# Performance work log

Hardware: AMD Instinct MI355X
Metric: run time of the kernel (lower is better)

## Reference

```python
import jax, jax.numpy as jnp
import numpy as np

HEADS = 8
DIM_HEAD = 128
BUCKET_SIZE = 128


def setup_inputs() -> dict:
    key = jax.random.key(0)
    ks = jax.random.split(key, 5)
    b, t, d = 4, 4096, 1024
    dh_all = HEADS * DIM_HEAD  # 1024
    x = jax.random.normal(ks[0], (b, t, d), dtype=jnp.float32)
    # 0.02 init scale keeps qk logits in a sane range (mimics trained-weight scale)
    Wq = jax.random.normal(ks[1], (d, dh_all), dtype=jnp.float32) * 0.02
    Wkv = jax.random.normal(ks[2], (d, 2 * dh_all), dtype=jnp.float32) * 0.02
    Wo = jax.random.normal(ks[3], (dh_all, d), dtype=jnp.float32) * 0.02
    bo = jnp.zeros((d,), dtype=jnp.float32)
    return {"x": x, "Wq": Wq, "Wkv": Wkv, "Wo": Wo, "bo": bo}


def reference(x, Wq, Wkv, Wo, bo):
    b, t, d = x.shape
    h, dh, bs = HEADS, DIM_HEAD, BUCKET_SIZE
    buckets = t // bs
    scale = dh ** -0.5

    # projections (Linear without bias for q/kv)
    q = x @ Wq                      # [b, t, h*dh]
    k, v = jnp.split(x @ Wkv, 2, axis=-1)

    def merge_heads(u):             # [b, t, h*dh] -> [b*h, t, dh]
        return u.reshape(b, t, h, dh).transpose(0, 2, 1, 3).reshape(b * h, t, dh)

    q, k, v = merge_heads(q), merge_heads(k), merge_heads(v)

    # bucket: [b*h, buckets, bs, dh]
    bq = q.reshape(b * h, buckets, bs, dh)
    bk = k.reshape(b * h, buckets, bs, dh)
    bv = v.reshape(b * h, buckets, bs, dh)

    # AttentionSortNet (non_permutative=True): bucket-mean similarity -> softmax
    sq = bq.mean(axis=2)            # [b*h, buckets, dh]
    sk = bk.mean(axis=2)
    R = jnp.einsum('bie,bje->bij', sq, sk) * scale
    R = jax.nn.softmax(R, axis=-1)  # [b*h, buckets, buckets]

    # soft-reorder kv buckets and concat with local buckets (n_sortcut == 0)
    bk_r = jnp.einsum('buv,bvtd->butd', R, bk)
    bv_r = jnp.einsum('buv,bvtd->butd', R, bv)
    bk_cat = jnp.concatenate([bk_r, bk], axis=2)   # [b*h, buckets, 2*bs, dh]
    bv_cat = jnp.concatenate([bv_r, bv], axis=2)

    # per-bucket attention
    dots = jnp.einsum('buie,buje->buij', bq, bk_cat) * scale
    attn = jax.nn.softmax(dots, axis=-1)
    out = jnp.einsum('buij,buje->buie', attn, bv_cat)  # [b*h, buckets, bs, dh]

    # unbucket + split heads back: [b, t, h*dh]
    out = out.reshape(b, h, t, dh).transpose(0, 2, 1, 3).reshape(b, t, h * dh)
    return out @ Wo + bo
```

## Files before the change

### kernel.cpp

```cpp
#include <hip/hip_runtime.h>
#include <hip/hip_bf16.h>
#include <stdint.h>

typedef short short8 __attribute__((ext_vector_type(8)));
typedef float f32x4 __attribute__((ext_vector_type(4)));
typedef float f32x2 __attribute__((ext_vector_type(2)));

__device__ __forceinline__ unsigned short f2bf(float f) {
    unsigned u = __float_as_uint(f);
    u += 0x7fff + ((u >> 16) & 1);
    return (unsigned short)(u >> 16);
}
__device__ __forceinline__ float bf2f(unsigned short h) {
    return __uint_as_float(((unsigned)h) << 16);
}

__device__ __forceinline__ void gload_lds16(const void* g, void* l) {
    __builtin_amdgcn_global_load_lds(
        (const __attribute__((address_space(1))) void*)g,
        (__attribute__((address_space(3))) void*)l, 16, 0, 0);
}

__global__ void cast_x_kernel(const float* __restrict__ x, unsigned short* __restrict__ xb, int n) {
    int i = (blockIdx.x * blockDim.x + threadIdx.x) * 4;
    int stride = gridDim.x * blockDim.x * 4;
    for (; i < n; i += stride) {
        float4 f = *(const float4*)(x + i);
        ushort4 o;
        o.x = f2bf(f.x); o.y = f2bf(f.y); o.z = f2bf(f.z); o.w = f2bf(f.w);
        *(ushort4*)(xb + i) = o;
    }
}

__global__ void transpose_cast_kernel(const float* __restrict__ W, unsigned short* __restrict__ Wt,
                                      int K, int N) {
    __shared__ unsigned short tile[32][33];
    int k0 = blockIdx.x * 32, n0 = blockIdx.y * 32;
    int tx = threadIdx.x & 31, ty = threadIdx.x >> 5;
#pragma unroll
    for (int i = 0; i < 32; i += 8)
        tile[ty + i][tx] = f2bf(W[(size_t)(k0 + ty + i) * N + n0 + tx]);
    __syncthreads();
#pragma unroll
    for (int i = 0; i < 32; i += 8)
        Wt[(size_t)(n0 + ty + i) * K + k0 + tx] = tile[tx][ty + i];
}

template <int MODE>
__global__ __launch_bounds__(512, 2)
void gemmP(const unsigned short* __restrict__ A, const unsigned short* __restrict__ B,
           unsigned short* __restrict__ obf, float* __restrict__ of,
           const float* __restrict__ bias) {
    __shared__ unsigned short Ssh[65536];
    const int tid = threadIdx.x;
    const int w = tid >> 6, lane = tid & 63;
    const int lr = lane & 15, lg = lane >> 4, r7 = lane & 7;
    const int wr = w >> 2, wc = w & 3;
    const int orig = blockIdx.x;
    const int lgc = (orig & 7) * 32 + (orig >> 3);
    const int m0 = (lgc >> 2) * 256, n0 = (lgc & 3) * 256;
    const int srow8 = lane >> 3;
    const int sgrp = (lane & 7) ^ srow8;
    const unsigned short* gA = A + (size_t)(m0 + w * 16 + srow8) * 1024 + sgrp * 8;
    const unsigned short* gB = B + (size_t)(n0 + w * 16 + srow8) * 1024 + sgrp * 8;

    f32x4 acc[8][4] = {};

#define SH(BUF, HALF, KT) {                                                              \
        const unsigned short* gp_ = ((HALF) < 2 ? gA : gB) +                             \
                                    (size_t)(((HALF) & 1) * 128) * 1024 + (KT);          \
        unsigned short* lp_ = Ssh + ((HALF) < 2 ? 0 : 32768) + (BUF) * 16384 +           \
                              ((HALF) & 1) * 8192 + w * 1024;                            \
        gload_lds16(gp_, lp_);                                                           \
        gload_lds16(gp_ + 8192, lp_ + 512);                                              \
    }

    SH(0, 0, 0) SH(0, 1, 0) SH(0, 2, 0) SH(0, 3, 0)
    SH(1, 0, 64) SH(1, 1, 64) SH(1, 2, 64) SH(1, 3, 64)
    asm volatile("s_waitcnt vmcnt(8)" ::: "memory");
    __builtin_amdgcn_sched_barrier(0);
    __builtin_amdgcn_s_barrier();

#pragma unroll 2
    for (int t = 0; t < 16; ++t) {
        const int cur = t & 1;
        const unsigned short* Ab = Ssh + cur * 16384;
        const unsigned short* Bb = Ssh + 32768 + cur * 16384;
        short8 af[8][2], bf[4][2];

#pragma unroll
        for (int mi = 0; mi < 4; ++mi)
#pragma unroll
            for (int kk = 0; kk < 2; ++kk)
                af[mi][kk] = *(const short8*)(Ab + (wr * 128 + mi * 16 + lr) * 64 +
                                              (((kk << 2) | lg) ^ r7) * 8);
#pragma unroll
        for (int ni = 0; ni < 2; ++ni)
#pragma unroll
            for (int kk = 0; kk < 2; ++kk)
                bf[ni][kk] = *(const short8*)(Bb + (wc * 64 + ni * 16 + lr) * 64 +
                                              (((kk << 2) | lg) ^ r7) * 8);
        __builtin_amdgcn_sched_barrier(0);
#pragma unroll
        for (int mi = 4; mi < 8; ++mi)
#pragma unroll
            for (int kk = 0; kk < 2; ++kk)
                af[mi][kk] = *(const short8*)(Ab + (wr * 128 + mi * 16 + lr) * 64 +
                                              (((kk << 2) | lg) ^ r7) * 8);
#pragma unroll
        for (int ni = 2; ni < 4; ++ni)
#pragma unroll
            for (int kk = 0; kk < 2; ++kk)
                bf[ni][kk] = *(const short8*)(Bb + (wc * 64 + ni * 16 + lr) * 64 +
                                              (((kk << 2) | lg) ^ r7) * 8);
        __builtin_amdgcn_sched_barrier(0);

        asm volatile("s_waitcnt lgkmcnt(12)" ::: "memory");
        __builtin_amdgcn_sched_barrier(0);
        __builtin_amdgcn_s_setprio(1);
#pragma unroll
        for (int mi = 0; mi < 4; ++mi)
#pragma unroll
            for (int ni = 0; ni < 2; ++ni)
#pragma unroll
                for (int kk = 0; kk < 2; ++kk)
                    acc[mi][ni] = __builtin_amdgcn_mfma_f32_16x16x32_bf16(af[mi][kk], bf[ni][kk],
                                                                          acc[mi][ni], 0, 0, 0);
        __builtin_amdgcn_s_setprio(0);

        asm volatile("s_waitcnt lgkmcnt(0)" ::: "memory");
        __builtin_amdgcn_sched_barrier(0);
        __builtin_amdgcn_s_barrier();
        if (t + 2 < 16) {
            const int kt2 = (t + 2) * 64;
            SH(cur, 0, kt2) SH(cur, 1, kt2) SH(cur, 2, kt2) SH(cur, 3, kt2)
        }

        __builtin_amdgcn_s_setprio(1);
#pragma unroll
        for (int mi = 4; mi < 8; ++mi)
#pragma unroll
            for (int ni = 0; ni < 2; ++ni)
#pragma unroll
                for (int kk = 0; kk < 2; ++kk)
                    acc[mi][ni] = __builtin_amdgcn_mfma_f32_16x16x32_bf16(af[mi][kk], bf[ni][kk],
                                                                          acc[mi][ni], 0, 0, 0);
#pragma unroll
        for (int mi = 0; mi < 8; ++mi)
#pragma unroll
            for (int ni = 2; ni < 4; ++ni)
#pragma unroll
                for (int kk = 0; kk < 2; ++kk)
                    acc[mi][ni] = __builtin_amdgcn_mfma_f32_16x16x32_bf16(af[mi][kk], bf[ni][kk],
                                                                          acc[mi][ni], 0, 0, 0);
        __builtin_amdgcn_s_setprio(0);

        if (t < 14) {
            asm volatile("s_waitcnt vmcnt(8)" ::: "memory");
            __builtin_amdgcn_sched_barrier(0);
        } else if (t == 14) {
            asm volatile("s_waitcnt vmcnt(0)" ::: "memory");
            __builtin_amdgcn_sched_barrier(0);
        }
        __builtin_amdgcn_s_barrier();
    }
#undef SH

#pragma unroll
    for (int mi = 0; mi < 8; ++mi)
#pragma unroll
        for (int ni = 0; ni < 4; ++ni) {
            if (MODE == 2) {
                int gm0 = m0 + wr * 128 + mi * 16 + lg * 4;
                int gn = n0 + wc * 64 + ni * 16 + lr;
                int b = gm0 >> 12, tt0 = gm0 & 4095, h = gn >> 7, dl = gn & 127;
                int u = tt0 >> 7, tl0 = tt0 & 127;
                size_t base = (size_t)(b * 8 + h) * 524288 + (size_t)u * 16384 + dl * 128 + tl0;
#pragma unroll
                for (int r = 0; r < 4; r += 2) {
                    unsigned pk = (unsigned)f2bf(acc[mi][ni][r]) |
                                  ((unsigned)f2bf(acc[mi][ni][r + 1]) << 16);
                    *(unsigned*)(obf + base + r) = pk;
                }
            } else {
#pragma unroll
                for (int r = 0; r < 4; ++r) {
                    int gm = m0 + wr * 128 + mi * 16 + lg * 4 + r;
                    int gn = n0 + wc * 64 + ni * 16 + lr;
                    float val = acc[mi][ni][r];
                    if (MODE == 3) {
                        of[(size_t)gm * 1024 + gn] = val + bias[gn];
                    } else {
                        int b = gm >> 12, tt = gm & 4095, h = gn >> 7, dl = gn & 127;
                        if (MODE == 0) {
                            obf[(size_t)(b * 8 + h) * 524288 + (size_t)tt * 128 + dl] =
                                f2bf(val * 0.08838834764831845f);
                        } else {
                            obf[(size_t)(b * 8 + h) * 524288 + (size_t)tt * 128 + dl] = f2bf(val);
                        }
                    }
                }
            }
        }

    if (MODE == 0 || MODE == 1) {
#pragma unroll
        for (int ni = 0; ni < 4; ++ni) {
            float ssum = 0.f;
#pragma unroll
            for (int mi = 0; mi < 8; ++mi)
#pragma unroll
                for (int r = 0; r < 4; ++r) ssum += acc[mi][ni][r];
            ssum += __shfl_xor(ssum, 16);
            ssum += __shfl_xor(ssum, 32);
            if (lane < 16) {
                int gn = n0 + wc * 64 + ni * 16 + lr;
                int h = gn >> 7, dl = gn & 127;
                int bh = (m0 >> 12) * 8 + h;
                int u = ((m0 & 4095) >> 7) + wr;
                const float sc = (MODE == 0) ? (0.08838834764831845f / 128.f) : (1.f / 128.f);
                of[(size_t)(bh * 32 + u) * 128 + dl] = ssum * sc;
            }
        }
    }
}

__global__ void sortnet_kernel(const float* __restrict__ sq, const float* __restrict__ sk,
                               float* __restrict__ R) {
    __shared__ float qs[32 * 129];
    __shared__ float ks[32 * 129];
    int bh = blockIdx.x, tid = threadIdx.x;
    for (int i = tid; i < 4096; i += 1024) {
        int row = i >> 7, col = i & 127;
        qs[row * 129 + col] = sq[(size_t)bh * 4096 + i];
        ks[row * 129 + col] = sk[(size_t)bh * 4096 + i];
    }
    __syncthreads();
    int u = tid >> 5, v = tid & 31;
    float dot = 0.f;
    for (int d = 0; d < 128; ++d) dot += qs[u * 129 + d] * ks[v * 129 + d];
    float mx = dot;
    for (int m = 16; m >= 1; m >>= 1) mx = fmaxf(mx, __shfl_xor(mx, m, 32));
    float e = __expf(dot - mx);
    float s = e;
    for (int m = 16; m >= 1; m >>= 1) s += __shfl_xor(s, m, 32);
    R[(size_t)bh * 1024 + u * 32 + v] = e / s;
}

__global__ __launch_bounds__(256, 4)
void mix_kernel(const unsigned short* __restrict__ k, const unsigned short* __restrict__ vT,
                const float* __restrict__ R, unsigned short* __restrict__ bkr,
                unsigned short* __restrict__ bvrT) {
    const int bid = blockIdx.x;
    const int arr = bid & 1;
    const int rest = bid >> 1;
    const int bh = rest >> 5, chunk = rest & 31;
    const int tid = threadIdx.x;
    const unsigned short* __restrict__ src = arr ? vT : k;
    unsigned short* __restrict__ dst = arr ? bvrT : bkr;
    const float* __restrict__ Rb = R + (size_t)bh * 1024;

    const int e = chunk * 512 + tid * 2;
    const size_t base = (size_t)bh * 524288 + e;

    unsigned raw[32];
#pragma unroll
    for (int vb = 0; vb < 32; ++vb)
        raw[vb] = *(const unsigned*)(src + base + (size_t)vb * 16384);
    f32x2 val[32];
#pragma unroll
    for (int vb = 0; vb < 32; ++vb)
        val[vb] = f32x2{bf2f((unsigned short)raw[vb]), bf2f((unsigned short)(raw[vb] >> 16))};

#pragma unroll 2
    for (int u = 0; u < 32; ++u) {
        f32x2 a0 = {0.f, 0.f}, a1 = {0.f, 0.f}, a2 = {0.f, 0.f}, a3 = {0.f, 0.f};
#pragma unroll
        for (int g = 0; g < 2; ++g) {
            float4 r0 = *(const float4*)(Rb + u * 32 + g * 16);
            float4 r1 = *(const float4*)(Rb + u * 32 + g * 16 + 4);
            float4 r2 = *(const float4*)(Rb + u * 32 + g * 16 + 8);
            float4 r3 = *(const float4*)(Rb + u * 32 + g * 16 + 12);
            const int b0 = g * 16;
            a0 += r0.x * val[b0 + 0];  a0 += r0.y * val[b0 + 1];
            a0 += r0.z * val[b0 + 2];  a0 += r0.w * val[b0 + 3];
            a1 += r1.x * val[b0 + 4];  a1 += r1.y * val[b0 + 5];
            a1 += r1.z * val[b0 + 6];  a1 += r1.w * val[b0 + 7];
            a2 += r2.x * val[b0 + 8];  a2 += r2.y * val[b0 + 9];
            a2 += r2.z * val[b0 + 10]; a2 += r2.w * val[b0 + 11];
            a3 += r3.x * val[b0 + 12]; a3 += r3.y * val[b0 + 13];
            a3 += r3.z * val[b0 + 14]; a3 += r3.w * val[b0 + 15];
        }
        f32x2 a = (a0 + a1) + (a2 + a3);
        unsigned o = (unsigned)f2bf(a.x) | ((unsigned)f2bf(a.y) << 16);
        *(unsigned*)(dst + (size_t)bh * 524288 + (size_t)u * 16384 + e) = o;
    }
}

__global__ __launch_bounds__(512)
void attn_kernel(const unsigned short* __restrict__ q, const unsigned short* __restrict__ k,
                 const unsigned short* __restrict__ vT, const unsigned short* __restrict__ bkr,
                 const unsigned short* __restrict__ bvrT, unsigned short* __restrict__ ao) {
    __shared__ unsigned short KB[2][8192];
    __shared__ unsigned short VB[2][8192];
    __shared__ unsigned short Ps[8][1024];
    const int orig = blockIdx.x;
    const int bid = (orig & 7) * 128 + (orig >> 3);
    const int bh = bid >> 5, u = bid & 31;
    const int tid = threadIdx.x, w = tid >> 6, lane = tid & 63;
    const int lr = lane & 15, lg = lane >> 4;
    const size_t bb = (size_t)bh * 524288 + (size_t)u * 16384;

#define STAGE_K(SRC, BUF)                                                        \
    _Pragma("unroll")                                                            \
    for (int i = 0; i < 2; ++i) {                                                \
        const int row_ = i * 32 + (tid >> 4);                                    \
        gload_lds16((SRC) + row_ * 128 + (((tid & 15) ^ (row_ & 7)) * 8),        \
                    (char*)KB[BUF] + i * 8192 + tid * 16);                       \
    }
#define STAGE_V(SRC, BUF)                                                        \
    _Pragma("unroll")                                                            \
    for (int i = 0; i < 2; ++i) {                                                \
        const int row_ = i * 64 + (tid >> 3);                                    \
        gload_lds16((SRC) + row_ * 128 + (((tid & 7) ^ (row_ & 7)) * 8),         \
                    (char*)VB[BUF] + i * 8192 + tid * 16);                       \
    }

    const unsigned short* qg = q + bb + (size_t)(w * 16) * 128;
    short8 aq[4];
#pragma unroll
    for (int kk = 0; kk < 4; ++kk)
        aq[kk] = *(const short8*)(qg + lr * 128 + kk * 32 + lg * 8);

    STAGE_K(bkr + bb, 0) STAGE_V(bvrT + bb, 0)
    STAGE_K(bkr + bb + 8192, 1) STAGE_V(bvrT + bb + 64, 1)

    short8 ones8;
#pragma unroll
    for (int i = 0; i < 8; ++i) ones8[i] = (short)0x3F80;

    f32x4 oacc[8] = {};
    f32x4 lacc = {};

    asm volatile("s_waitcnt vmcnt(4)" ::: "memory");
    __builtin_amdgcn_sched_barrier(0);
    __builtin_amdgcn_s_barrier();

    unsigned short* Pw = Ps[w];

#pragma unroll
    for (int c = 0; c < 4; ++c) {
        const int cb = c & 1;
        f32x4 s[4] = {};
        __builtin_amdgcn_s_setprio(1);
#pragma unroll
        for (int kk = 0; kk < 4; ++kk)
#pragma unroll
            for (int ni = 0; ni < 4; ++ni) {
                short8 kb8 = *(const short8*)(&KB[cb][(ni * 16 + lr) * 128 +
                                              (((kk * 4 + lg) ^ (lr & 7)) * 8)]);
                s[ni] = __builtin_amdgcn_mfma_f32_16x16x32_bf16(aq[kk], kb8, s[ni], 0, 0, 0);
            }
        __builtin_amdgcn_s_setprio(0);

#pragma unroll
        for (int r = 0; r < 4; ++r) {
            int prow = lg * 4 + r;
#pragma unroll
            for (int ni = 0; ni < 4; ++ni)
                Pw[prow * 64 + ((ni * 16 + lr) ^ ((prow & 7) << 3))] = f2bf(__expf(s[ni][r]));
        }

        __builtin_amdgcn_s_setprio(1);
#pragma unroll
        for (int ks2 = 0; ks2 < 2; ++ks2) {
            short8 ap = *(const short8*)(&Pw[lr * 64 + ((ks2 * 32 + lg * 8) ^ ((lr & 7) << 3))]);
            lacc = __builtin_amdgcn_mfma_f32_16x16x32_bf16(ap, ones8, lacc, 0, 0, 0);
#pragma unroll
            for (int ni = 0; ni < 8; ++ni) {
                short8 bv8 = *(const short8*)(&VB[cb][(ni * 16 + lr) * 64 +
                                              (((ks2 * 4 + lg) ^ (lr & 7)) * 8)]);
                oacc[ni] = __builtin_amdgcn_mfma_f32_16x16x32_bf16(ap, bv8, oacc[ni], 0, 0, 0);
            }
        }
        __builtin_amdgcn_s_setprio(0);

        __builtin_amdgcn_s_barrier();
        if (c == 0) { STAGE_K(k + bb, 0) STAGE_V(vT + bb, 0) }
        else if (c == 1) { STAGE_K(k + bb + 8192, 1) STAGE_V(vT + bb + 64, 1) }
        if (c < 2) {
            asm volatile("s_waitcnt vmcnt(4)" ::: "memory");
            __builtin_amdgcn_sched_barrier(0);
            __builtin_amdgcn_s_barrier();
        } else if (c == 2) {
            asm volatile("s_waitcnt vmcnt(0)" ::: "memory");
            __builtin_amdgcn_sched_barrier(0);
            __builtin_amdgcn_s_barrier();
        }
    }

    const int b = bh >> 3, h = bh & 7;
#pragma unroll
    for (int r = 0; r < 4; ++r) {
        int row = w * 16 + lg * 4 + r;
        size_t rowbase = ((size_t)b * 4096 + u * 128 + row) * 1024 + h * 128;
        float inv = 1.f / lacc[r];
#pragma unroll
        for (int ni = 0; ni < 8; ++ni)
            ao[rowbase + ni * 16 + lr] = f2bf(oacc[ni][r] * inv);
    }
#undef STAGE_K
#undef STAGE_V
}

extern "C" void kernel_launch(void* const* d_in, const int* in_sizes, int n_in,
                              void* d_out, int out_size, void* d_ws, size_t ws_size,
                              hipStream_t stream) {
    (void)in_sizes; (void)n_in; (void)out_size; (void)ws_size;
    const float* x   = (const float*)d_in[0];
    const float* Wq  = (const float*)d_in[1];
    const float* Wkv = (const float*)d_in[2];
    const float* Wo  = (const float*)d_in[3];
    const float* bo  = (const float*)d_in[4];
    float* out = (float*)d_out;

    char* ws = (char*)d_ws;
    const size_t SZ_BIG = 33554432;
    unsigned short* xb    = (unsigned short*)(ws);
    unsigned short* qb    = (unsigned short*)(ws + SZ_BIG);
    unsigned short* kb    = (unsigned short*)(ws + 2 * SZ_BIG);
    unsigned short* vtb   = (unsigned short*)(ws + 3 * SZ_BIG);
    unsigned short* bkr   = (unsigned short*)(ws + 4 * SZ_BIG);
    unsigned short* bvrT  = (unsigned short*)(ws + 5 * SZ_BIG);
    size_t off = 6 * SZ_BIG;
    unsigned short* wqkvt = (unsigned short*)(ws + off); off += 6291456;
    unsigned short* wot   = (unsigned short*)(ws + off); off += 2097152;
    float* sq   = (float*)(ws + off); off += 524288;
    float* sk   = (float*)(ws + off); off += 524288;
    float* Rbuf = (float*)(ws + off); off += 131072;

    cast_x_kernel<<<4096, 256, 0, stream>>>(x, xb, 16777216);
    transpose_cast_kernel<<<dim3(32, 32), 256, 0, stream>>>(Wq, wqkvt, 1024, 1024);
    transpose_cast_kernel<<<dim3(32, 64), 256, 0, stream>>>(Wkv, wqkvt + 1048576, 1024, 2048);
    transpose_cast_kernel<<<dim3(32, 32), 256, 0, stream>>>(Wo, wot, 1024, 1024);

    gemmP<0><<<256, 512, 0, stream>>>(xb, wqkvt,           qb,  sq, nullptr);
    gemmP<1><<<256, 512, 0, stream>>>(xb, wqkvt + 1048576, kb,  sk, nullptr);
    gemmP<2><<<256, 512, 0, stream>>>(xb, wqkvt + 2097152, vtb, nullptr, nullptr);

    sortnet_kernel<<<32, 1024, 0, stream>>>(sq, sk, Rbuf);
    mix_kernel<<<2048, 256, 0, stream>>>(kb, vtb, Rbuf, bkr, bvrT);

    attn_kernel<<<1024, 512, 0, stream>>>(qb, kb, vtb, bkr, bvrT, xb);

    gemmP<3><<<256, 512, 0, stream>>>(xb, wot, nullptr, out, bo);
}
```

Before: 262.0 us.

## Interleave GEMM LDS prefetch quarters with MFMA sub-blocks in four-phase loop

Restructures the projection GEMM main loop into four phases. Each phase issues one quarter of the global-to-LDS prefetch, loads part of the fragments and runs one MFMA quadrant, with barriers between phases. The last B quarter of the next tile is now issued inside the current iteration rather than in the prologue. The goal is to spread global-load issue across the compute so memory traffic overlaps MFMA work more evenly, at the cost of more barriers and more complex vmcnt accounting.

```diff
diff --git a/kernel.cpp b/kernel.cpp
--- a/kernel.cpp
+++ b/kernel.cpp
@@ -76,8 +76,8 @@
     }
 
     SH(0, 0, 0) SH(0, 1, 0) SH(0, 2, 0) SH(0, 3, 0)
-    SH(1, 0, 64) SH(1, 1, 64) SH(1, 2, 64) SH(1, 3, 64)
-    asm volatile("s_waitcnt vmcnt(8)" ::: "memory");
+    SH(1, 0, 64) SH(1, 1, 64) SH(1, 2, 64)
+    asm volatile("s_waitcnt vmcnt(6)" ::: "memory");
     __builtin_amdgcn_sched_barrier(0);
     __builtin_amdgcn_s_barrier();
 
@@ -86,6 +86,7 @@
         const int cur = t & 1;
         const unsigned short* Ab = Ssh + cur * 16384;
         const unsigned short* Bb = Ssh + 32768 + cur * 16384;
+        const int kt1 = (t + 1) * 64, kt2 = (t + 2) * 64;
         short8 af[8][2], bf[4][2];
 
 #pragma unroll
@@ -100,69 +101,92 @@
             for (int kk = 0; kk < 2; ++kk)
                 bf[ni][kk] = *(const short8*)(Bb + (wc * 64 + ni * 16 + lr) * 64 +
                                               (((kk << 2) | lg) ^ r7) * 8);
+        if (t + 1 < 16) { SH(cur ^ 1, 3, kt1) }
+        asm volatile("s_waitcnt lgkmcnt(8)" ::: "memory");
         __builtin_amdgcn_sched_barrier(0);
+        __builtin_amdgcn_s_barrier();
+        asm volatile("s_waitcnt lgkmcnt(0)" ::: "memory");
+        __builtin_amdgcn_sched_barrier(0);
+        __builtin_amdgcn_s_setprio(1);
+#pragma unroll
+        for (int mi = 0; mi < 4; ++mi)
+#pragma unroll
+            for (int ni = 0; ni < 2; ++ni)
+#pragma unroll
+                for (int kk = 0; kk < 2; ++kk)
+                    acc[mi][ni] = __builtin_amdgcn_mfma_f32_16x16x32_bf16(af[mi][kk], bf[ni][kk],
+                                                                          acc[mi][ni], 0, 0, 0);
+        __builtin_amdgcn_s_setprio(0);
+        __builtin_amdgcn_s_barrier();
+
 #pragma unroll
         for (int mi = 4; mi < 8; ++mi)
 #pragma unroll
             for (int kk = 0; kk < 2; ++kk)
                 af[mi][kk] = *(const short8*)(Ab + (wr * 128 + mi * 16 + lr) * 64 +
                                               (((kk << 2) | lg) ^ r7) * 8);
+        if (t + 2 < 16) { SH(cur, 0, kt2) }
+        __builtin_amdgcn_s_barrier();
+        asm volatile("s_waitcnt lgkmcnt(0)" ::: "memory");
+        __builtin_amdgcn_sched_barrier(0);
+        __builtin_amdgcn_s_setprio(1);
+#pragma unroll
+        for (int mi = 4; mi < 8; ++mi)
+#pragma unroll
+            for (int ni = 0; ni < 2; ++ni)
+#pragma unroll
+                for (int kk = 0; kk < 2; ++kk)
+                    acc[mi][ni] = __builtin_amdgcn_mfma_f32_16x16x32_bf16(af[mi][kk], bf[ni][kk],
+                                                                          acc[mi][ni], 0, 0, 0);
+        __builtin_amdgcn_s_setprio(0);
+        __builtin_amdgcn_s_barrier();
+
 #pragma unroll
         for (int ni = 2; ni < 4; ++ni)
 #pragma unroll
             for (int kk = 0; kk < 2; ++kk)
                 bf[ni][kk] = *(const short8*)(Bb + (wc * 64 + ni * 16 + lr) * 64 +
                                               (((kk << 2) | lg) ^ r7) * 8);
+        if (t + 2 < 16) { SH(cur, 1, kt2) }
+        __builtin_amdgcn_s_barrier();
+        asm volatile("s_waitcnt lgkmcnt(0)" ::: "memory");
         __builtin_amdgcn_sched_barrier(0);
-
-        asm volatile("s_waitcnt lgkmcnt(12)" ::: "memory");
-        __builtin_amdgcn_sched_barrier(0);
-        __builtin_amdgcn_s_setprio(1);
-#pragma unroll
-        for (int mi = 0; mi < 4; ++mi)
-#pragma unroll
-            for (int ni = 0; ni < 2; ++ni)
+        __builtin_amdgcn_s_setprio(1);
+#pragma unroll
+        for (int mi = 4; mi < 8; ++mi)
+#pragma unroll
+            for (int ni = 2; ni < 4; ++ni)
 #pragma unroll
                 for (int kk = 0; kk < 2; ++kk)
                     acc[mi][ni] = __builtin_amdgcn_mfma_f32_16x16x32_bf16(af[mi][kk], bf[ni][kk],
                                                                           acc[mi][ni], 0, 0, 0);
         __builtin_amdgcn_s_setprio(0);
-
-        asm volatile("s_waitcnt lgkmcnt(0)" ::: "memory");
-        __builtin_amdgcn_sched_barrier(0);
-        __builtin_amdgcn_s_barrier();
-        if (t + 2 < 16) {
-            const int kt2 = (t + 2) * 64;
-            SH(cur, 0, kt2) SH(cur, 1, kt2) SH(cur, 2, kt2) SH(cur, 3, kt2)
-        }
-
-        __builtin_amdgcn_s_setprio(1);
-#pragma unroll
-        for (int mi = 4; mi < 8; ++mi)
-#pragma unroll
-            for (int ni = 0; ni < 2; ++ni)
+        __builtin_amdgcn_s_barrier();
+
+        if (t + 2 < 16) { SH(cur, 2, kt2) }
+        __builtin_amdgcn_s_setprio(1);
+#pragma unroll
+        for (int mi = 0; mi < 4; ++mi)
+#pragma unroll
+            for (int ni = 2; ni < 4; ++ni)
 #pragma unroll
                 for (int kk = 0; kk < 2; ++kk)
                     acc[mi][ni] = __builtin_amdgcn_mfma_f32_16x16x32_bf16(af[mi][kk], bf[ni][kk],
                                                                           acc[mi][ni], 0, 0, 0);
-#pragma unroll
-        for (int mi = 0; mi < 8; ++mi)
-#pragma unroll
-            for (int ni = 2; ni < 4; ++ni)
-#pragma unroll
-                for (int kk = 0; kk < 2; ++kk)
-                    acc[mi][ni] = __builtin_amdgcn_mfma_f32_16x16x32_bf16(af[mi][kk], bf[ni][kk],
-                                                                          acc[mi][ni], 0, 0, 0);
-        __builtin_amdgcn_s_setprio(0);
-
-        if (t < 14) {
-            asm volatile("s_waitcnt vmcnt(8)" ::: "memory");
+        __builtin_amdgcn_s_setprio(0);
+        if (t < 13) {
+            asm volatile("s_waitcnt vmcnt(6)" ::: "memory");
             __builtin_amdgcn_sched_barrier(0);
+            __builtin_amdgcn_s_barrier();
+        } else if (t == 13) {
+            asm volatile("s_waitcnt vmcnt(6)" ::: "memory");
+            __builtin_amdgcn_sched_barrier(0);
+            __builtin_amdgcn_s_barrier();
         } else if (t == 14) {
             asm volatile("s_waitcnt vmcnt(0)" ::: "memory");
             __builtin_amdgcn_sched_barrier(0);
-        }
-        __builtin_amdgcn_s_barrier();
+            __builtin_amdgcn_s_barrier();
+        }
     }
 #undef SH
 
```

Result: no change. 261.8 us (-0.0%).
